# Kernel tuning notes

Measured on AMD Instinct MI355X. Metric: run time of the kernel, lower is better.

The kernel has to match this reference:

```python
import jax, jax.numpy as jnp
import numpy as np
import math

S, H, NH, HD = 2048, 1280, 16, 80
WIN = 64
NW = S // WIN
I = 3420
OUT = 3584
L = 8
FULL_IDX = (3, 7)
MERGE = 4  # spatial_merge_size**2
EPS = 1e-6


def setup_inputs() -> dict:
    key = jax.random.key(0)
    ks = jax.random.split(key, 16)
    w = lambda k, s: jax.random.normal(k, s, jnp.float32) * 0.02
    # rotary tables: half-dim freqs duplicated, as in Qwen2.5-VL vision rotary
    inv_freq = 1.0 / (10000.0 ** (np.arange(0, HD // 2, dtype=np.float32) / (HD // 2)))
    freqs = np.outer(np.arange(S, dtype=np.float32), inv_freq)  # [S, HD/2]
    emb = np.concatenate([freqs, freqs], axis=-1)               # [S, HD]
    return {
        "hidden_states": jax.random.normal(ks[0], (S, H), jnp.float32),
        "full_attn_masks": jnp.ones((1, 1, S, S), jnp.float32),
        "window_attn_masks": jnp.ones((NW, 1, WIN, WIN), jnp.float32),
        "cos": jnp.asarray(np.cos(emb)),
        "sin": jnp.asarray(np.sin(emb)),
        "qkv_w": w(ks[1], (L, 3 * H, H)),
        "qkv_b": w(ks[2], (L, 3 * H)),
        "proj_w": w(ks[3], (L, H, H)),
        "proj_b": w(ks[4], (L, H)),
        "norm1_w": jnp.ones((L, H), jnp.float32),
        "norm2_w": jnp.ones((L, H), jnp.float32),
        "gate_w": w(ks[5], (L, I, H)),
        "gate_b": w(ks[6], (L, I)),
        "up_w": w(ks[7], (L, I, H)),
        "up_b": w(ks[8], (L, I)),
        "down_w": w(ks[9], (L, H, I)),
        "down_b": w(ks[10], (L, H)),
        "ln_q_w": jnp.ones((H,), jnp.float32),
        "m0_w": w(ks[11], (H * MERGE, H * MERGE)),
        "m0_b": w(ks[12], (H * MERGE,)),
        "m2_w": w(ks[13], (OUT, H * MERGE)),
        "m2_b": w(ks[14], (OUT,)),
    }


def rmsnorm(x, w):
    v = jnp.mean(jnp.square(x.astype(jnp.float32)), axis=-1, keepdims=True)
    return (x * jax.lax.rsqrt(v + EPS)) * w


def rotate_half(x):
    x1, x2 = jnp.split(x, 2, axis=-1)
    return jnp.concatenate([-x2, x1], axis=-1)


def apply_rope(q, k, cos, sin):
    return q * cos + rotate_half(q) * sin, k * cos + rotate_half(k) * sin


def attn_full(x, mask, cos, sin, qkv_w, qkv_b, proj_w, proj_b):
    # x: [S, H]; mask: [1, 1, S, S] (additive)
    qkv = (x @ qkv_w.T + qkv_b).reshape(S, 3, NH, HD)
    q, k, v = [t[:, i].transpose(1, 0, 2) for i, t in [(0, qkv), (1, qkv), (2, qkv)]]  # [NH, S, HD]
    q, k = apply_rope(q, k, cos, sin)  # cos/sin [S, HD] broadcast over heads
    aw = jnp.einsum('hsd,htd->hst', q, k) / math.sqrt(HD) + mask[0]
    aw = jax.nn.softmax(aw.astype(jnp.float32), axis=-1)
    o = jnp.einsum('hst,htd->hsd', aw, v).transpose(1, 0, 2).reshape(S, NH * HD)
    return o @ proj_w.T + proj_b


def attn_window(x, mask, cos, sin, qkv_w, qkv_b, proj_w, proj_b):
    xw = x.reshape(NW, WIN, H)
    qkv = (xw @ qkv_w.T + qkv_b).reshape(NW, WIN, 3, NH, HD).transpose(2, 0, 3, 1, 4)
    q, k, v = qkv[0], qkv[1], qkv[2]
    cw = cos.reshape(NW, 1, WIN, HD)
    sw = sin.reshape(NW, 1, WIN, HD)
    q, k = apply_rope(q, k, cw, sw)
    aw = jnp.einsum('whsd,whtd->whst', q, k) / math.sqrt(HD) + mask
    aw = jax.nn.softmax(aw.astype(jnp.float32), axis=-1)
    o = jnp.einsum('whst,whtd->whsd', aw, v).transpose(0, 2, 1, 3).reshape(S, NH * HD)
    return o @ proj_w.T + proj_b


def reference(hidden_states, full_attn_masks, window_attn_masks, cos, sin,
              qkv_w, qkv_b, proj_w, proj_b, norm1_w, norm2_w,
              gate_w, gate_b, up_w, up_b, down_w, down_b,
              ln_q_w, m0_w, m0_b, m2_w, m2_b):
    NEG = jnp.finfo(jnp.float32).min
    fm = (1.0 - full_attn_masks) * NEG
    wm = (1.0 - window_attn_masks) * NEG
    x = hidden_states
    for i in range(L):
        h = rmsnorm(x, norm1_w[i])
        if i in FULL_IDX:
            a = attn_full(h, fm, cos, sin, qkv_w[i], qkv_b[i], proj_w[i], proj_b[i])
        else:
            a = attn_window(h, wm, cos, sin, qkv_w[i], qkv_b[i], proj_w[i], proj_b[i])
        x = x + a
        h = rmsnorm(x, norm2_w[i])
        mlp = (jax.nn.silu(h @ gate_w[i].T + gate_b[i]) * (h @ up_w[i].T + up_b[i])) @ down_w[i].T + down_b[i]
        x = x + mlp
    # patch merger: RMSNorm -> merge 4 tokens -> Linear-GELU-Linear
    h = rmsnorm(x, ln_q_w).reshape(-1, H * MERGE)  # [S/4, 5120]
    h = jax.nn.gelu(h @ m0_w.T + m0_b, approximate=False)
    return h @ m2_w.T + m2_b  # [S/4, OUT]
```

## Files before the change

kernel.cpp:

```cpp
#include <hip/hip_runtime.h>
#include <hip/hip_bf16.h>
#include <math.h>

#define S_LEN 2048
#define HID   1280
#define NHEADS 16
#define HDIM  80
#define HDP   96
#define VROWS 96
#define LAYERS 8
#define IDIM  3420
#define IDIMP 3456
#define MERGED 5120
#define OUTD  3584
#define NCH   8
#define CHLEN 256
#define LWE   19824640LL

typedef __attribute__((ext_vector_type(8))) short short8;
typedef __attribute__((ext_vector_type(4))) float f32x4;
typedef __attribute__((ext_vector_type(16))) float f32x16;
typedef unsigned int u32;
typedef __attribute__((ext_vector_type(4))) u32 u32x4;
typedef __attribute__((address_space(1))) const u32* gptr_t;
typedef __attribute__((address_space(3))) u32* lptr_t;

__device__ inline unsigned short f2b(float f){
  __hip_bfloat16 b = __float2bfloat16(f);
  return __builtin_bit_cast(unsigned short, b);
}
__device__ inline float b2f(unsigned short u){
  return __bfloat162float(__builtin_bit_cast(__hip_bfloat16, u));
}
__device__ inline unsigned pk2(float lo, float hi){
  return (unsigned)f2b(lo) | ((unsigned)f2b(hi) << 16);
}

#define NSEG 42
struct ConvSegs {
  unsigned long long gpre[NSEG + 1];
  long long srcoff[NSEG];
  long long dstoff[NSEG];
  int srcbase[NSEG];
  int N[NSEG], K[NSEG], Np[NSEG], Kp[NSEG];
};

__global__ __launch_bounds__(256) void convert_all_kernel(
    ConvSegs cs,
    const float* __restrict__ b0, const float* __restrict__ b1,
    const float* __restrict__ b2, const float* __restrict__ b3,
    const float* __restrict__ b4, const float* __restrict__ b5,
    const float* __restrict__ b6,
    unsigned short* __restrict__ dst)
{
  size_t total = cs.gpre[NSEG];
  for (size_t i = (size_t)blockIdx.x * 256 + threadIdx.x; i < total;
       i += (size_t)gridDim.x * 256){
    int lo = 0, hi = NSEG - 1;
    while (lo < hi){ int mid = (lo + hi + 1) >> 1;
      if (cs.gpre[mid] <= i) lo = mid; else hi = mid - 1; }
    size_t g = i - cs.gpre[lo];
    int Kp = cs.Kp[lo], K = cs.K[lo], N = cs.N[lo];
    int kg = Kp >> 3;
    int k8 = (int)(g % kg);
    int n  = (int)(g / kg);
    int k0 = k8 * 8;
    const float* base;
    switch (cs.srcbase[lo]){
      case 0: base = b0; break; case 1: base = b1; break;
      case 2: base = b2; break; case 3: base = b3; break;
      case 4: base = b4; break; case 5: base = b5; break;
      default: base = b6; break;
    }
    const float* src = base + cs.srcoff[lo];
    u32 out[4];
    if (n < N && k0 + 8 <= K){
      const float* s = src + (size_t)n * K + k0;
      float4 f0 = *(const float4*)s;
      float4 f1 = *(const float4*)(s + 4);
      out[0] = pk2(f0.x, f0.y); out[1] = pk2(f0.z, f0.w);
      out[2] = pk2(f1.x, f1.y); out[3] = pk2(f1.z, f1.w);
    } else {
      #pragma unroll
      for (int j = 0; j < 4; ++j){
        int ka = k0 + 2 * j;
        float lv = (n < N && ka     < K) ? src[(size_t)n * K + ka]     : 0.f;
        float hv = (n < N && ka + 1 < K) ? src[(size_t)n * K + ka + 1] : 0.f;
        out[j] = pk2(lv, hv);
      }
    }
    *(uint4*)(dst + cs.dstoff[lo] + g * 8) = make_uint4(out[0], out[1], out[2], out[3]);
  }
}

__global__ __launch_bounds__(256) void concat_bias_kernel(
    const float* __restrict__ g, const float* __restrict__ u, float* __restrict__ o)
{
  int L = blockIdx.y;
  int n = blockIdx.x * 256 + threadIdx.x;
  if (n >= 2 * IDIMP) return;
  float* ol = o + (size_t)L * 2 * IDIMP;
  const float* gl = g + (size_t)L * IDIM;
  const float* ul = u + (size_t)L * IDIM;
  if (n < IDIMP) ol[n] = (n < IDIM) ? gl[n] : 0.f;
  else { int m2 = n - IDIMP; ol[n] = (m2 < IDIM) ? ul[m2] : 0.f; }
}

__global__ __launch_bounds__(256) void rmsnorm_kernel(
    const float* __restrict__ x, const float* __restrict__ w,
    unsigned short* __restrict__ out, int H)
{
  int s = blockIdx.x;
  const float* row = x + (size_t)s * H;
  float ss = 0.f;
  for (int c = threadIdx.x; c < H; c += 256){ float v = row[c]; ss += v * v; }
  #pragma unroll
  for (int off = 32; off >= 1; off >>= 1) ss += __shfl_xor(ss, off, 64);
  __shared__ float red[4];
  if ((threadIdx.x & 63) == 0) red[threadIdx.x >> 6] = ss;
  __syncthreads();
  ss = red[0] + red[1] + red[2] + red[3];
  float rs = rsqrtf(ss / H + 1e-6f);
  unsigned short* orow = out + (size_t)s * H;
  for (int c = threadIdx.x; c < H; c += 256) orow[c] = f2b(row[c] * rs * w[c]);
}

template<int EPI, int BM>
__global__ __launch_bounds__(256) void gemm_kernel(
    const unsigned short* __restrict__ A, int lda,
    const unsigned short* __restrict__ B, int ldb,
    const float* __restrict__ bias, int Nact,
    void* __restrict__ Cv, int ldc,
    const float* __restrict__ res,
    int K)
{
  constexpr int MI = BM / 32;
  __shared__ __align__(16) unsigned short As[2][BM * 32];
  __shared__ __align__(16) unsigned short Bs[2][4096];
  const int tid  = threadIdx.x;
  const int lane = tid & 63;
  const int wave = tid >> 6;
  const int wm = wave >> 1, wn = wave & 1;
  const int m0 = blockIdx.y * BM, n0 = blockIdx.x * 128;
  const int l16 = lane & 15, lh = lane >> 4;
  const int lrow = lane >> 2;
  const int lcol = lane & 3;
  f32x4 acc[MI][4] = {};

  auto stage = [&](int bufi, int k0){
    #pragma unroll
    for (int j = 0; j < BM / 64; ++j){
      int chunk = wave * (BM / 64) + j;
      int row  = chunk * 16 + lrow;
      int slot = lcol ^ ((row >> 1) & 3);
      const unsigned short* srcA = A + (size_t)(m0 + row) * lda + k0 + slot * 8;
      __builtin_amdgcn_global_load_lds((gptr_t)srcA, (lptr_t)&As[bufi][chunk * 512], 16, 0, 0);
    }
    #pragma unroll
    for (int j = 0; j < 2; ++j){
      int chunk = wave * 2 + j;
      int row  = chunk * 16 + lrow;
      int slot = lcol ^ ((row >> 1) & 3);
      const unsigned short* srcB = B + (size_t)(n0 + row) * ldb + k0 + slot * 8;
      __builtin_amdgcn_global_load_lds((gptr_t)srcB, (lptr_t)&Bs[bufi][chunk * 512], 16, 0, 0);
    }
  };

  const int nt = K >> 5;
  stage(0, 0);
  __syncthreads();
  int buf = 0;
  for (int t = 0; t < nt; ++t){
    if (t + 1 < nt) stage(buf ^ 1, (t + 1) << 5);
    short8 af[MI], bfr[4];
    #pragma unroll
    for (int mi = 0; mi < MI; ++mi){
      int r = wm * (BM / 2) + mi * 16 + l16;
      int sl = lh ^ ((r >> 1) & 3);
      af[mi] = *(const short8*)&As[buf][r * 32 + sl * 8];
    }
    #pragma unroll
    for (int ni = 0; ni < 4; ++ni){
      int r = wn * 64 + ni * 16 + l16;
      int sl = lh ^ ((r >> 1) & 3);
      bfr[ni] = *(const short8*)&Bs[buf][r * 32 + sl * 8];
    }
    #pragma unroll
    for (int mi = 0; mi < MI; ++mi)
      #pragma unroll
      for (int ni = 0; ni < 4; ++ni)
        acc[mi][ni] = __builtin_amdgcn_mfma_f32_16x16x32_bf16(af[mi], bfr[ni], acc[mi][ni], 0, 0, 0);
    __syncthreads();
    buf ^= 1;
  }

  #pragma unroll
  for (int mi = 0; mi < MI; ++mi){
    int row = m0 + wm * (BM / 2) + mi * 16 + lh * 4;
    #pragma unroll
    for (int ni = 0; ni < 4; ++ni){
      int gn = n0 + wn * 64 + ni * 16 + l16;
      float bv = (gn < Nact) ? bias[gn] : 0.f;
      #pragma unroll
      for (int r2 = 0; r2 < 4; ++r2){
        float v = acc[mi][ni][r2] + bv;
        size_t offc = (size_t)(row + r2) * ldc + gn;
        if (EPI == 0)      ((float*)Cv)[offc] = v;
        else if (EPI == 1) ((float*)Cv)[offc] = res[offc] + v;
        else if (EPI == 2) ((unsigned short*)Cv)[offc] = f2b(0.5f * v * (1.0f + erff(v * 0.70710678118f)));
        else               ((unsigned short*)Cv)[offc] = f2b(v);
      }
    }
  }
}

__global__ __launch_bounds__(256) void rope_split_kernel(
    const unsigned short* __restrict__ qkv, const float* __restrict__ cosT,
    const float* __restrict__ sinT,
    unsigned short* __restrict__ qo, unsigned short* __restrict__ ko,
    unsigned short* __restrict__ vt)
{
  __shared__ unsigned short vtile[80][128];
  const int h = blockIdx.x;
  const int s0 = blockIdx.y * 128;
  const int t = threadIdx.x;
  const int sr = t >> 1, half = t & 1;
  const int s = s0 + sr;
  const unsigned short* row = qkv + (size_t)s * 3840 + h * 80;
  const float* crow = cosT + (size_t)s * 80;
  const float* srow = sinT + (size_t)s * 80;
  const float sgn = half ? 1.f : -1.f;
  #pragma unroll
  for (int g = 0; g < 5; ++g){
    int d  = half * 40 + g * 8;
    int dp = 40 - half * 40 + g * 8;
    short8 q8  = *(const short8*)(row + d);
    short8 k8  = *(const short8*)(row + 1280 + d);
    short8 qp8 = *(const short8*)(row + dp);
    short8 kp8 = *(const short8*)(row + 1280 + dp);
    short8 v8  = *(const short8*)(row + 2560 + d);
    float4 c0  = *(const float4*)(crow + d);
    float4 c1  = *(const float4*)(crow + d + 4);
    float4 sn0 = *(const float4*)(srow + d);
    float4 sn1 = *(const float4*)(srow + d + 4);
    float cc[8] = {c0.x, c0.y, c0.z, c0.w, c1.x, c1.y, c1.z, c1.w};
    float ss[8] = {sn0.x, sn0.y, sn0.z, sn0.w, sn1.x, sn1.y, sn1.z, sn1.w};
    short8 qo8, ko8;
    #pragma unroll
    for (int j = 0; j < 8; ++j){
      float qv = b2f((unsigned short)q8[j]);
      float kv = b2f((unsigned short)k8[j]);
      float qr = sgn * b2f((unsigned short)qp8[j]);
      float kr = sgn * b2f((unsigned short)kp8[j]);
      qo8[j] = (short)f2b(qv * cc[j] + qr * ss[j]);
      ko8[j] = (short)f2b(kv * cc[j] + kr * ss[j]);
      vtile[d + j][sr] = (unsigned short)v8[j];
    }
    size_t qkoff = ((size_t)h * S_LEN + s) * HDP + d;
    *(short8*)(qo + qkoff) = qo8;
    *(short8*)(ko + qkoff) = ko8;
  }
  {
    short8 z = {};
    size_t poff = ((size_t)h * S_LEN + s) * HDP + 80 + half * 8;
    *(short8*)(qo + poff) = z;
    *(short8*)(ko + poff) = z;
  }
  __syncthreads();
  #pragma unroll
  for (int it = 0; it < 5; ++it){
    int j = t + it * 256;
    int d = j >> 4, ch = j & 15;
    uint4 v = *(const uint4*)&vtile[d][ch * 8];
    *(uint4*)(vt + ((size_t)h * VROWS + d) * S_LEN + s0 + ch * 8) = v;
  }
}

template<int PART>
__global__ __launch_bounds__(256) void flash_kernel(
    const unsigned short* __restrict__ q, const unsigned short* __restrict__ k,
    const unsigned short* __restrict__ vt, unsigned short* __restrict__ out,
    float* __restrict__ opart, float* __restrict__ mlpart)
{
  __shared__ unsigned short ot[4][32][88];
  const int lane = threadIdx.x & 63;
  const int w = threadIdx.x >> 6;
  const int h = blockIdx.y;
  const int l31 = lane & 31, lh1 = lane >> 5;
  const int qr = blockIdx.x * 128 + w * 32;
  const int ch = PART ? blockIdx.z : 0;
  const unsigned short* qh = q + (size_t)h * S_LEN * HDP;
  const unsigned short* kh = k + (size_t)h * S_LEN * HDP;
  const unsigned short* vh = vt + (size_t)h * VROWS * S_LEN;

  short8 qa[5];
  #pragma unroll
  for (int kc = 0; kc < 5; ++kc)
    qa[kc] = *(const short8*)(qh + (size_t)(qr + l31) * HDP + kc * 16 + lh1 * 8);

  float m_ = -1e30f, l_ = 0.f;
  f32x16 o0 = {}, o1 = {}, o2 = {};
  const int kvb = PART ? ch * CHLEN : (qr & ~63);
  const int kve = PART ? ch * CHLEN + CHLEN : (qr & ~63) + 64;
  const float scale = 0.11180339887498949f;

  for (int kvt = kvb; kvt < kve; kvt += 32){
    f32x16 sc = {};
    __builtin_amdgcn_s_setprio(1);
    #pragma unroll
    for (int kc = 0; kc < 5; ++kc){
      short8 kf = *(const short8*)(kh + (size_t)(kvt + l31) * HDP + kc * 16 + lh1 * 8);
      sc = __builtin_amdgcn_mfma_f32_32x32x16_bf16(kf, qa[kc], sc, 0, 0, 0);
    }
    __builtin_amdgcn_s_setprio(0);
    float t = sc[0];
    #pragma unroll
    for (int i = 1; i < 16; ++i) t = fmaxf(t, sc[i]);
    t = fmaxf(t, __shfl_xor(t, 32)) * scale;
    if (!__all(t <= m_ + 8.f)){
      float mnew = fmaxf(m_, t);
      float corr = __expf(m_ - mnew);
      l_ *= corr;
      #pragma unroll
      for (int i = 0; i < 16; ++i){ o0[i] *= corr; o1[i] *= corr; o2[i] *= corr; }
      m_ = mnew;
    }
    float p[16];
    float rs = 0.f;
    #pragma unroll
    for (int i = 0; i < 16; ++i){ p[i] = __expf(sc[i] * scale - m_); rs += p[i]; }
    rs += __shfl_xor(rs, 32);
    l_ += rs;
    unsigned wd0[4], wd1[4];
    #pragma unroll
    for (int j = 0; j < 2; ++j){
      unsigned Aj = pk2(p[2 * j],     p[2 * j + 1]);
      unsigned Bj = pk2(p[4 + 2 * j], p[4 + 2 * j + 1]);
      unsigned t0 = __shfl_xor(Aj, 32);
      unsigned t1 = __shfl_xor(Bj, 32);
      wd0[j]     = lh1 ? t1 : Aj;
      wd0[2 + j] = lh1 ? Bj : t0;
      Aj = pk2(p[8 + 2 * j],  p[8 + 2 * j + 1]);
      Bj = pk2(p[12 + 2 * j], p[12 + 2 * j + 1]);
      t0 = __shfl_xor(Aj, 32);
      t1 = __shfl_xor(Bj, 32);
      wd1[j]     = lh1 ? t1 : Aj;
      wd1[2 + j] = lh1 ? Bj : t0;
    }
    __builtin_amdgcn_s_setprio(1);
    #pragma unroll
    for (int kc2 = 0; kc2 < 2; ++kc2){
      u32x4 uw = kc2 ? u32x4{wd1[0], wd1[1], wd1[2], wd1[3]}
                     : u32x4{wd0[0], wd0[1], wd0[2], wd0[3]};
      short8 pb = __builtin_bit_cast(short8, uw);
      const unsigned short* vb = vh + kvt + kc2 * 16 + lh1 * 8;
      o0 = __builtin_amdgcn_mfma_f32_32x32x16_bf16(
          *(const short8*)(vb + (size_t)(l31)      * S_LEN), pb, o0, 0, 0, 0);
      o1 = __builtin_amdgcn_mfma_f32_32x32x16_bf16(
          *(const short8*)(vb + (size_t)(32 + l31) * S_LEN), pb, o1, 0, 0, 0);
      o2 = __builtin_amdgcn_mfma_f32_32x32x16_bf16(
          *(const short8*)(vb + (size_t)(64 + l31) * S_LEN), pb, o2, 0, 0, 0);
    }
    __builtin_amdgcn_s_setprio(0);
  }

  if (PART){
    const size_t hb = (size_t)(ch * NHEADS + h) * 80;
    #pragma unroll
    for (int r = 0; r < 16; ++r){
      int dl = (r & 3) + 8 * (r >> 2) + 4 * lh1;
      opart[(hb + dl)      * S_LEN + qr + l31] = o0[r];
      opart[(hb + 32 + dl) * S_LEN + qr + l31] = o1[r];
      if (dl < 16) opart[(hb + 64 + dl) * S_LEN + qr + l31] = o2[r];
    }
    if (lane < 32){
      size_t mb = ((size_t)(ch * NHEADS + h) * S_LEN + qr + l31) * 2;
      mlpart[mb] = m_; mlpart[mb + 1] = l_;
    }
  } else {
    float inv = 1.f / l_;
    #pragma unroll
    for (int r = 0; r < 16; ++r){
      int dl = (r & 3) + 8 * (r >> 2) + 4 * lh1;
      ot[w][l31][dl]      = f2b(o0[r] * inv);
      ot[w][l31][32 + dl] = f2b(o1[r] * inv);
      if (dl < 16) ot[w][l31][64 + dl] = f2b(o2[r] * inv);
    }
    int qq = lane >> 1, half = lane & 1;
    #pragma unroll
    for (int j = 0; j < 20; ++j){
      unsigned v = *(const unsigned*)&ot[w][qq][half * 40 + j * 2];
      *(unsigned*)&out[(size_t)(qr + qq) * HID + h * HDIM + half * 40 + j * 2] = v;
    }
  }
}

__global__ __launch_bounds__(256) void flash_reduce_kernel(
    const float* __restrict__ opart, const float* __restrict__ mlpart,
    unsigned short* __restrict__ out)
{
  __shared__ float wn[NCH][256];
  __shared__ unsigned short ot[256][82];
  const int tid = threadIdx.x;
  const int h = blockIdx.y;
  const int q0 = blockIdx.x * 256;
  float mv[NCH], lv[NCH];
  float M = -1e30f;
  #pragma unroll
  for (int c = 0; c < NCH; ++c){
    size_t mb = ((size_t)(c * NHEADS + h) * S_LEN + q0 + tid) * 2;
    mv[c] = mlpart[mb]; lv[c] = mlpart[mb + 1];
    M = fmaxf(M, mv[c]);
  }
  float L = 0.f;
  #pragma unroll
  for (int c = 0; c < NCH; ++c){ mv[c] = __expf(mv[c] - M); L += mv[c] * lv[c]; }
  float invL = 1.f / L;
  #pragma unroll
  for (int c = 0; c < NCH; ++c) wn[c][tid] = mv[c] * invL;
  __syncthreads();
  for (int d = 0; d < HDIM; ++d){
    float acc = 0.f;
    #pragma unroll
    for (int c = 0; c < NCH; ++c)
      acc += wn[c][tid] * opart[((size_t)(c * NHEADS + h) * 80 + d) * S_LEN + q0 + tid];
    ot[tid][d] = f2b(acc);
  }
  __syncthreads();
  #pragma unroll
  for (int j = 0; j < 40; ++j){
    unsigned v = *(const unsigned*)&ot[tid][j * 2];
    *(unsigned*)&out[(size_t)(q0 + tid) * HID + h * HDIM + j * 2] = v;
  }
}

__global__ __launch_bounds__(256) void silu_mul_kernel(
    const unsigned short* __restrict__ gu, unsigned short* __restrict__ out)
{
  size_t i = ((size_t)blockIdx.x * 256 + threadIdx.x) * 8;
  if (i >= (size_t)S_LEN * IDIMP) return;
  int row = (int)(i / IDIMP), col = (int)(i % IDIMP);
  short8 g8 = *(const short8*)(gu + (size_t)row * (2 * IDIMP) + col);
  short8 u8 = *(const short8*)(gu + (size_t)row * (2 * IDIMP) + IDIMP + col);
  short8 o8;
  #pragma unroll
  for (int j = 0; j < 8; ++j){
    float gv = b2f((unsigned short)g8[j]);
    float uv = b2f((unsigned short)u8[j]);
    o8[j] = (short)f2b(gv / (1.f + __expf(-gv)) * uv);
  }
  *(short8*)(out + i) = o8;
}

extern "C" void kernel_launch(void* const* d_in, const int* in_sizes, int n_in,
                              void* d_out, int out_size, void* d_ws, size_t ws_size,
                              hipStream_t stream)
{
  const float* hidden = (const float*)d_in[0];
  const float* cosT   = (const float*)d_in[3];
  const float* sinT   = (const float*)d_in[4];
  const float* qkv_w  = (const float*)d_in[5];
  const float* qkv_b  = (const float*)d_in[6];
  const float* proj_w = (const float*)d_in[7];
  const float* proj_b = (const float*)d_in[8];
  const float* norm1_w= (const float*)d_in[9];
  const float* norm2_w= (const float*)d_in[10];
  const float* gate_w = (const float*)d_in[11];
  const float* gate_b = (const float*)d_in[12];
  const float* up_w   = (const float*)d_in[13];
  const float* up_b   = (const float*)d_in[14];
  const float* down_w = (const float*)d_in[15];
  const float* down_b = (const float*)d_in[16];
  const float* ln_q_w = (const float*)d_in[17];
  const float* m0_w   = (const float*)d_in[18];
  const float* m0_b   = (const float*)d_in[19];
  const float* m2_w   = (const float*)d_in[20];
  const float* m2_b   = (const float*)d_in[21];

  char* ws = (char*)d_ws;
  size_t off = 0;
  auto carve = [&](size_t bytes)->char*{
    char* p = ws + off; off += (bytes + 255) & ~(size_t)255; return p;
  };
  float*          x    = (float*)         carve((size_t)S_LEN * HID * 4);
  unsigned short* hbuf = (unsigned short*)carve((size_t)S_LEN * HID * 2);
  unsigned short* qkvb = (unsigned short*)carve((size_t)S_LEN * 3840 * 2);
  unsigned short* qp   = (unsigned short*)carve((size_t)NHEADS * S_LEN * HDP * 2);
  unsigned short* kp   = (unsigned short*)carve((size_t)NHEADS * S_LEN * HDP * 2);
  unsigned short* vtb  = (unsigned short*)carve((size_t)NHEADS * VROWS * S_LEN * 2);
  unsigned short* ao   = (unsigned short*)carve((size_t)S_LEN * HID * 2);
  unsigned short* gbuf = (unsigned short*)carve((size_t)S_LEN * 2 * IDIMP * 2);
  unsigned short* mlp  = (unsigned short*)carve((size_t)S_LEN * IDIMP * 2);
  unsigned short* mg   = (unsigned short*)carve((size_t)512 * MERGED * 2);
  float*          opart= (float*)         carve((size_t)NCH * NHEADS * 80 * S_LEN * 4);
  float*          mlpt = (float*)         carve((size_t)NCH * NHEADS * S_LEN * 2 * 4);
  float*          cbias= (float*)         carve((size_t)LAYERS * 2 * IDIMP * 4);
  unsigned short* wbf  = (unsigned short*)carve((size_t)203161600 * 2);
  (void)ws_size; (void)in_sizes; (void)n_in; (void)out_size;

  ConvSegs cs;
  {
    unsigned long long g = 0; int si = 0;
    auto add = [&](int base, long long soff, long long doff, int N, int K, int Np, int Kp){
      cs.gpre[si] = g; cs.srcbase[si] = base; cs.srcoff[si] = soff; cs.dstoff[si] = doff;
      cs.N[si] = N; cs.K[si] = K; cs.Np[si] = Np; cs.Kp[si] = Kp;
      g += (unsigned long long)Np * (Kp >> 3); ++si;
    };
    for (long long i = 0; i < LAYERS; ++i){
      add(0, i * 3840LL * HID, i * LWE + 0,        3840, HID, 3840, HID);
      add(1, i * (long long)HID * HID, i * LWE + 4915200,  HID, HID, HID, HID);
      add(2, i * (long long)IDIM * HID, i * LWE + 6553600,  IDIM, HID, IDIMP, HID);
      add(3, i * (long long)IDIM * HID, i * LWE + 10977280, IDIM, HID, IDIMP, HID);
      add(4, i * (long long)HID * IDIM, i * LWE + 15400960, HID, IDIM, HID, IDIMP);
    }
    add(5, 0, 8 * LWE,            MERGED, MERGED, MERGED, MERGED);
    add(6, 0, 8 * LWE + 26214400, OUTD,   MERGED, OUTD,   MERGED);
    cs.gpre[NSEG] = g;
  }

  convert_all_kernel<<<4096, 256, 0, stream>>>(
      cs, qkv_w, proj_w, gate_w, up_w, down_w, m0_w, m2_w, wbf);
  concat_bias_kernel<<<dim3(27, LAYERS), 256, 0, stream>>>(gate_b, up_b, cbias);
  hipMemcpyAsync(x, hidden, (size_t)S_LEN * HID * 4, hipMemcpyDeviceToDevice, stream);

  for (int i = 0; i < LAYERS; ++i){
    unsigned short* wl = wbf + (size_t)i * LWE;
    unsigned short* wqkv = wl;
    unsigned short* wproj= wl + 4915200;
    unsigned short* wgate= wl + 6553600;
    unsigned short* wdown= wl + 15400960;

    rmsnorm_kernel<<<S_LEN, 256, 0, stream>>>(x, norm1_w + (size_t)i * HID, hbuf, HID);
    gemm_kernel<3,128><<<dim3(30, 16), 256, 0, stream>>>(
        hbuf, HID, wqkv, HID, qkv_b + (size_t)i * 3840, 3840,
        qkvb, 3840, nullptr, HID);
    rope_split_kernel<<<dim3(NHEADS, 16), 256, 0, stream>>>(qkvb, cosT, sinT, qp, kp, vtb);
    if (i == 3 || i == 7){
      flash_kernel<1><<<dim3(16, 16, NCH), 256, 0, stream>>>(qp, kp, vtb, nullptr, opart, mlpt);
      flash_reduce_kernel<<<dim3(8, 16), 256, 0, stream>>>(opart, mlpt, ao);
    } else {
      flash_kernel<0><<<dim3(16, 16), 256, 0, stream>>>(qp, kp, vtb, ao, nullptr, nullptr);
    }
    gemm_kernel<1,64><<<dim3(10, 32), 256, 0, stream>>>(
        ao, HID, wproj, HID, proj_b + (size_t)i * HID, HID,
        x, HID, x, HID);
    rmsnorm_kernel<<<S_LEN, 256, 0, stream>>>(x, norm2_w + (size_t)i * HID, hbuf, HID);
    gemm_kernel<3,128><<<dim3(54, 16), 256, 0, stream>>>(
        hbuf, HID, wgate, HID, cbias + (size_t)i * 2 * IDIMP, 2 * IDIMP,
        gbuf, 2 * IDIMP, nullptr, HID);
    silu_mul_kernel<<<(int)(((size_t)S_LEN * IDIMP / 8 + 255) / 256), 256, 0, stream>>>(gbuf, mlp);
    gemm_kernel<1,64><<<dim3(10, 32), 256, 0, stream>>>(
        mlp, IDIMP, wdown, IDIMP, down_b + (size_t)i * HID, HID,
        x, HID, x, IDIMP);
  }
  unsigned short* wm0 = wbf + 8 * LWE;
  unsigned short* wm2 = wm0 + (size_t)MERGED * MERGED;
  rmsnorm_kernel<<<S_LEN, 256, 0, stream>>>(x, ln_q_w, hbuf, HID);
  gemm_kernel<2,64><<<dim3(40, 8), 256, 0, stream>>>(
      hbuf, MERGED, wm0, MERGED, m0_b, MERGED, mg, MERGED, nullptr, MERGED);
  gemm_kernel<0,64><<<dim3(28, 8), 256, 0, stream>>>(
      mg, MERGED, wm2, MERGED, m2_b, OUTD, d_out, OUTD, nullptr, MERGED);
}
```

Baseline: 2.753 ms.

## Interleave gate/up weights and fuse SiLU-multiply into the gate/up GEMM epilogue

Weight conversion now interleaves gate and up rows, so each adjacent output column pair is (gate, up). A new GEMM epilogue swaps partners with a lane shuffle and writes silu(g)*u directly as bf16. This removes the separate silu_mul kernel and the round trip of the 2x-wide intermediate buffer. The conversion kernel is also restructured to one element per thread with per-block segment lookup and nontemporal loads and stores. Half the lanes idle during the epilogue store.

```diff
diff --git a/kernel.cpp b/kernel.cpp
--- a/kernel.cpp
+++ b/kernel.cpp
@@ -38,11 +38,12 @@
 
 #define NSEG 42
 struct ConvSegs {
-  unsigned long long gpre[NSEG + 1];
+  int bpre[NSEG + 1];
   long long srcoff[NSEG];
   long long dstoff[NSEG];
   int srcbase[NSEG];
-  int N[NSEG], K[NSEG], Np[NSEG], Kp[NSEG];
+  int N[NSEG], K[NSEG], Kp[NSEG];
+  int rstride[NSEG], roffs[NSEG];
 };
 
 __global__ __launch_bounds__(256) void convert_all_kernel(
@@ -53,44 +54,45 @@
     const float* __restrict__ b6,
     unsigned short* __restrict__ dst)
 {
-  size_t total = cs.gpre[NSEG];
-  for (size_t i = (size_t)blockIdx.x * 256 + threadIdx.x; i < total;
-       i += (size_t)gridDim.x * 256){
-    int lo = 0, hi = NSEG - 1;
-    while (lo < hi){ int mid = (lo + hi + 1) >> 1;
-      if (cs.gpre[mid] <= i) lo = mid; else hi = mid - 1; }
-    size_t g = i - cs.gpre[lo];
-    int Kp = cs.Kp[lo], K = cs.K[lo], N = cs.N[lo];
-    int kg = Kp >> 3;
-    int k8 = (int)(g % kg);
-    int n  = (int)(g / kg);
-    int k0 = k8 * 8;
-    const float* base;
-    switch (cs.srcbase[lo]){
-      case 0: base = b0; break; case 1: base = b1; break;
-      case 2: base = b2; break; case 3: base = b3; break;
-      case 4: base = b4; break; case 5: base = b5; break;
-      default: base = b6; break;
-    }
-    const float* src = base + cs.srcoff[lo];
-    u32 out[4];
-    if (n < N && k0 + 8 <= K){
-      const float* s = src + (size_t)n * K + k0;
-      float4 f0 = *(const float4*)s;
-      float4 f1 = *(const float4*)(s + 4);
-      out[0] = pk2(f0.x, f0.y); out[1] = pk2(f0.z, f0.w);
-      out[2] = pk2(f1.x, f1.y); out[3] = pk2(f1.z, f1.w);
-    } else {
-      #pragma unroll
-      for (int j = 0; j < 4; ++j){
-        int ka = k0 + 2 * j;
-        float lv = (n < N && ka     < K) ? src[(size_t)n * K + ka]     : 0.f;
-        float hv = (n < N && ka + 1 < K) ? src[(size_t)n * K + ka + 1] : 0.f;
-        out[j] = pk2(lv, hv);
-      }
-    }
-    *(uint4*)(dst + cs.dstoff[lo] + g * 8) = make_uint4(out[0], out[1], out[2], out[3]);
-  }
+  const int b = blockIdx.x;
+  int seg = 0;
+  while (seg < NSEG - 1 && cs.bpre[seg + 1] <= b) ++seg;
+  const int Kp = cs.Kp[seg], K = cs.K[seg], N = cs.N[seg];
+  const int kg = Kp >> 3;
+  size_t g = (size_t)(b - cs.bpre[seg]) * 256 + threadIdx.x;
+  int k8 = (int)(g % kg);
+  int n  = (int)(g / kg);
+  int k0 = k8 * 8;
+  const float* base;
+  switch (cs.srcbase[seg]){
+    case 0: base = b0; break; case 1: base = b1; break;
+    case 2: base = b2; break; case 3: base = b3; break;
+    case 4: base = b4; break; case 5: base = b5; break;
+    default: base = b6; break;
+  }
+  const float* src = base + cs.srcoff[seg];
+  u32 out0, out1, out2, out3;
+  if (n < N && k0 + 8 <= K){
+    const float* s = src + (size_t)n * K + k0;
+    f32x4 f0 = __builtin_nontemporal_load((const f32x4*)s);
+    f32x4 f1 = __builtin_nontemporal_load((const f32x4*)(s + 4));
+    out0 = pk2(f0[0], f0[1]); out1 = pk2(f0[2], f0[3]);
+    out2 = pk2(f1[0], f1[1]); out3 = pk2(f1[2], f1[3]);
+  } else {
+    u32 tmp[4];
+    #pragma unroll
+    for (int j = 0; j < 4; ++j){
+      int ka = k0 + 2 * j;
+      float lv = (n < N && ka     < K) ? src[(size_t)n * K + ka]     : 0.f;
+      float hv = (n < N && ka + 1 < K) ? src[(size_t)n * K + ka + 1] : 0.f;
+      tmp[j] = pk2(lv, hv);
+    }
+    out0 = tmp[0]; out1 = tmp[1]; out2 = tmp[2]; out3 = tmp[3];
+  }
+  size_t de = (size_t)cs.dstoff[seg] +
+              ((size_t)n * cs.rstride[seg] + cs.roffs[seg]) * Kp + k0;
+  u32x4 ov = {out0, out1, out2, out3};
+  __builtin_nontemporal_store(ov, (u32x4*)(dst + de));
 }
 
 __global__ __launch_bounds__(256) void concat_bias_kernel(
@@ -99,11 +101,10 @@
   int L = blockIdx.y;
   int n = blockIdx.x * 256 + threadIdx.x;
   if (n >= 2 * IDIMP) return;
-  float* ol = o + (size_t)L * 2 * IDIMP;
-  const float* gl = g + (size_t)L * IDIM;
-  const float* ul = u + (size_t)L * IDIM;
-  if (n < IDIMP) ol[n] = (n < IDIM) ? gl[n] : 0.f;
-  else { int m2 = n - IDIMP; ol[n] = (m2 < IDIM) ? ul[m2] : 0.f; }
+  int c = n >> 1, which = n & 1;
+  float v = 0.f;
+  if (c < IDIM) v = which ? u[(size_t)L * IDIM + c] : g[(size_t)L * IDIM + c];
+  o[(size_t)L * 2 * IDIMP + n] = v;
 }
 
 __global__ __launch_bounds__(256) void rmsnorm_kernel(
@@ -204,11 +205,19 @@
       #pragma unroll
       for (int r2 = 0; r2 < 4; ++r2){
         float v = acc[mi][ni][r2] + bv;
-        size_t offc = (size_t)(row + r2) * ldc + gn;
-        if (EPI == 0)      ((float*)Cv)[offc] = v;
-        else if (EPI == 1) ((float*)Cv)[offc] = res[offc] + v;
-        else if (EPI == 2) ((unsigned short*)Cv)[offc] = f2b(0.5f * v * (1.0f + erff(v * 0.70710678118f)));
-        else               ((unsigned short*)Cv)[offc] = f2b(v);
+        if (EPI == 4){
+          float partner = __shfl_xor(v, 1);
+          if (!(l16 & 1)){
+            float r = v / (1.f + __expf(-v)) * partner;
+            ((unsigned short*)Cv)[(size_t)(row + r2) * ldc + (gn >> 1)] = f2b(r);
+          }
+        } else {
+          size_t offc = (size_t)(row + r2) * ldc + gn;
+          if (EPI == 0)      ((float*)Cv)[offc] = v;
+          else if (EPI == 1) ((float*)Cv)[offc] = res[offc] + v;
+          else if (EPI == 2) ((unsigned short*)Cv)[offc] = f2b(0.5f * v * (1.0f + erff(v * 0.70710678118f)));
+          else               ((unsigned short*)Cv)[offc] = f2b(v);
+        }
       }
     }
   }
@@ -239,12 +248,12 @@
     short8 qp8 = *(const short8*)(row + dp);
     short8 kp8 = *(const short8*)(row + 1280 + dp);
     short8 v8  = *(const short8*)(row + 2560 + d);
-    float4 c0  = *(const float4*)(crow + d);
-    float4 c1  = *(const float4*)(crow + d + 4);
-    float4 sn0 = *(const float4*)(srow + d);
-    float4 sn1 = *(const float4*)(srow + d + 4);
-    float cc[8] = {c0.x, c0.y, c0.z, c0.w, c1.x, c1.y, c1.z, c1.w};
-    float ss[8] = {sn0.x, sn0.y, sn0.z, sn0.w, sn1.x, sn1.y, sn1.z, sn1.w};
+    f32x4 c0  = *(const f32x4*)(crow + d);
+    f32x4 c1  = *(const f32x4*)(crow + d + 4);
+    f32x4 sn0 = *(const f32x4*)(srow + d);
+    f32x4 sn1 = *(const f32x4*)(srow + d + 4);
+    float cc[8] = {c0[0], c0[1], c0[2], c0[3], c1[0], c1[1], c1[2], c1[3]};
+    float ss[8] = {sn0[0], sn0[1], sn0[2], sn0[3], sn1[0], sn1[1], sn1[2], sn1[3]};
     short8 qo8, ko8;
     #pragma unroll
     for (int j = 0; j < 8; ++j){
@@ -271,8 +280,8 @@
   for (int it = 0; it < 5; ++it){
     int j = t + it * 256;
     int d = j >> 4, ch = j & 15;
-    uint4 v = *(const uint4*)&vtile[d][ch * 8];
-    *(uint4*)(vt + ((size_t)h * VROWS + d) * S_LEN + s0 + ch * 8) = v;
+    u32x4 v = *(const u32x4*)&vtile[d][ch * 8];
+    *(u32x4*)(vt + ((size_t)h * VROWS + d) * S_LEN + s0 + ch * 8) = v;
   }
 }
 
@@ -432,24 +441,6 @@
     unsigned v = *(const unsigned*)&ot[tid][j * 2];
     *(unsigned*)&out[(size_t)(q0 + tid) * HID + h * HDIM + j * 2] = v;
   }
-}
-
-__global__ __launch_bounds__(256) void silu_mul_kernel(
-    const unsigned short* __restrict__ gu, unsigned short* __restrict__ out)
-{
-  size_t i = ((size_t)blockIdx.x * 256 + threadIdx.x) * 8;
-  if (i >= (size_t)S_LEN * IDIMP) return;
-  int row = (int)(i / IDIMP), col = (int)(i % IDIMP);
-  short8 g8 = *(const short8*)(gu + (size_t)row * (2 * IDIMP) + col);
-  short8 u8 = *(const short8*)(gu + (size_t)row * (2 * IDIMP) + IDIMP + col);
-  short8 o8;
-  #pragma unroll
-  for (int j = 0; j < 8; ++j){
-    float gv = b2f((unsigned short)g8[j]);
-    float uv = b2f((unsigned short)u8[j]);
-    o8[j] = (short)f2b(gv / (1.f + __expf(-gv)) * uv);
-  }
-  *(short8*)(out + i) = o8;
 }
 
 extern "C" void kernel_launch(void* const* d_in, const int* in_sizes, int n_in,
@@ -489,7 +480,6 @@
   unsigned short* kp   = (unsigned short*)carve((size_t)NHEADS * S_LEN * HDP * 2);
   unsigned short* vtb  = (unsigned short*)carve((size_t)NHEADS * VROWS * S_LEN * 2);
   unsigned short* ao   = (unsigned short*)carve((size_t)S_LEN * HID * 2);
-  unsigned short* gbuf = (unsigned short*)carve((size_t)S_LEN * 2 * IDIMP * 2);
   unsigned short* mlp  = (unsigned short*)carve((size_t)S_LEN * IDIMP * 2);
   unsigned short* mg   = (unsigned short*)carve((size_t)512 * MERGED * 2);
   float*          opart= (float*)         carve((size_t)NCH * NHEADS * 80 * S_LEN * 4);
@@ -499,26 +489,32 @@
   (void)ws_size; (void)in_sizes; (void)n_in; (void)out_size;
 
   ConvSegs cs;
+  int totalblocks = 0;
   {
-    unsigned long long g = 0; int si = 0;
-    auto add = [&](int base, long long soff, long long doff, int N, int K, int Np, int Kp){
-      cs.gpre[si] = g; cs.srcbase[si] = base; cs.srcoff[si] = soff; cs.dstoff[si] = doff;
-      cs.N[si] = N; cs.K[si] = K; cs.Np[si] = Np; cs.Kp[si] = Kp;
-      g += (unsigned long long)Np * (Kp >> 3); ++si;
+    int si = 0;
+    auto add = [&](int base, long long soff, long long doff, int N, int K,
+                   int Np, int Kp, int rstride, int roffs){
+      cs.bpre[si] = totalblocks;
+      cs.srcbase[si] = base; cs.srcoff[si] = soff; cs.dstoff[si] = doff;
+      cs.N[si] = N; cs.K[si] = K; cs.Kp[si] = Kp;
+      cs.rstride[si] = rstride; cs.roffs[si] = roffs;
+      long long groups = (long long)Np * (Kp >> 3);
+      totalblocks += (int)((groups + 255) / 256);
+      ++si;
     };
     for (long long i = 0; i < LAYERS; ++i){
-      add(0, i * 3840LL * HID, i * LWE + 0,        3840, HID, 3840, HID);
-      add(1, i * (long long)HID * HID, i * LWE + 4915200,  HID, HID, HID, HID);
-      add(2, i * (long long)IDIM * HID, i * LWE + 6553600,  IDIM, HID, IDIMP, HID);
-      add(3, i * (long long)IDIM * HID, i * LWE + 10977280, IDIM, HID, IDIMP, HID);
-      add(4, i * (long long)HID * IDIM, i * LWE + 15400960, HID, IDIM, HID, IDIMP);
-    }
-    add(5, 0, 8 * LWE,            MERGED, MERGED, MERGED, MERGED);
-    add(6, 0, 8 * LWE + 26214400, OUTD,   MERGED, OUTD,   MERGED);
-    cs.gpre[NSEG] = g;
-  }
-
-  convert_all_kernel<<<4096, 256, 0, stream>>>(
+      add(0, i * 3840LL * HID,        i * LWE + 0,        3840, HID, 3840, HID, 1, 0);
+      add(1, i * (long long)HID * HID, i * LWE + 4915200,  HID, HID, HID, HID, 1, 0);
+      add(2, i * (long long)IDIM * HID, i * LWE + 6553600,  IDIM, HID, IDIMP, HID, 2, 0);
+      add(3, i * (long long)IDIM * HID, i * LWE + 6553600,  IDIM, HID, IDIMP, HID, 2, 1);
+      add(4, i * (long long)HID * IDIM, i * LWE + 15400960, HID, IDIM, HID, IDIMP, 1, 0);
+    }
+    add(5, 0, 8 * LWE,            MERGED, MERGED, MERGED, MERGED, 1, 0);
+    add(6, 0, 8 * LWE + 26214400, OUTD,   MERGED, OUTD,   MERGED, 1, 0);
+    cs.bpre[NSEG] = totalblocks;
+  }
+
+  convert_all_kernel<<<totalblocks, 256, 0, stream>>>(
       cs, qkv_w, proj_w, gate_w, up_w, down_w, m0_w, m2_w, wbf);
   concat_bias_kernel<<<dim3(27, LAYERS), 256, 0, stream>>>(gate_b, up_b, cbias);
   hipMemcpyAsync(x, hidden, (size_t)S_LEN * HID * 4, hipMemcpyDeviceToDevice, stream);
@@ -527,7 +523,7 @@
     unsigned short* wl = wbf + (size_t)i * LWE;
     unsigned short* wqkv = wl;
     unsigned short* wproj= wl + 4915200;
-    unsigned short* wgate= wl + 6553600;
+    unsigned short* wgu  = wl + 6553600;
     unsigned short* wdown= wl + 15400960;
 
     rmsnorm_kernel<<<S_LEN, 256, 0, stream>>>(x, norm1_w + (size_t)i * HID, hbuf, HID);
@@ -545,10 +541,9 @@
         ao, HID, wproj, HID, proj_b + (size_t)i * HID, HID,
         x, HID, x, HID);
     rmsnorm_kernel<<<S_LEN, 256, 0, stream>>>(x, norm2_w + (size_t)i * HID, hbuf, HID);
-    gemm_kernel<3,128><<<dim3(54, 16), 256, 0, stream>>>(
-        hbuf, HID, wgate, HID, cbias + (size_t)i * 2 * IDIMP, 2 * IDIMP,
-        gbuf, 2 * IDIMP, nullptr, HID);
-    silu_mul_kernel<<<(int)(((size_t)S_LEN * IDIMP / 8 + 255) / 256), 256, 0, stream>>>(gbuf, mlp);
+    gemm_kernel<4,128><<<dim3(54, 16), 256, 0, stream>>>(
+        hbuf, HID, wgu, HID, cbias + (size_t)i * 2 * IDIMP, 2 * IDIMP,
+        mlp, IDIMP, nullptr, HID);
     gemm_kernel<1,64><<<dim3(10, 32), 256, 0, stream>>>(
         mlp, IDIMP, wdown, IDIMP, down_b + (size_t)i * HID, HID,
         x, HID, x, IDIMP);
```

New measurement: 2.593 ms. -5.8%, faster.
